# Kernel optimization log

Hardware: AMD Instinct MI355X
Metric: run time of the kernel (lower is better)

Reference implementation:

```python
import jax, jax.numpy as jnp
import numpy as np

K = 4  # recurrent_kernel_size


def setup_inputs() -> dict:
    key = jax.random.key(0)
    k1, k2, k3, k4 = jax.random.split(key, 4)
    b, t, d = 4, 4096, 1024
    x = jax.random.normal(k1, (b, t, d), dtype=jnp.float32)
    W_conv = jax.random.normal(k2, (d, 1, K), dtype=jnp.float32) * (1.0 / np.sqrt(K))
    W_proj = jax.random.normal(k3, (4 * d, d), dtype=jnp.float32) * (1.0 / np.sqrt(d))
    W_out = jax.random.normal(k4, (d, d), dtype=jnp.float32) * (1.0 / np.sqrt(d))
    return {"x": x, "W_conv": W_conv, "W_proj": W_proj, "W_out": W_out}


def _causal_dwconv(x_btd, W_conv):
    # x: [b,t,d]; W_conv: [d,1,k] (torch depthwise layout). Causal: left-pad k-1.
    d = x_btd.shape[-1]
    x_bdt = jnp.transpose(x_btd, (0, 2, 1))  # [b,d,t]
    y = jax.lax.conv_general_dilated(
        x_bdt, W_conv,
        window_strides=(1,),
        padding=[(K - 1, 0)],
        feature_group_count=d,
        dimension_numbers=("NCH", "OIH", "NCH"),
    )
    return jnp.transpose(y, (0, 2, 1))  # [b,t,d]


def reference(x, W_conv, W_proj, W_out):
    b, t, d = x.shape
    mixed = _causal_dwconv(x, W_conv)
    u = jnp.einsum("btd,ed->bte", x + mixed, W_proj)  # [b,t,4d]
    v, gate, decay, inject = jnp.split(u, 4, axis=-1)
    gate = jax.nn.sigmoid(gate)
    decay = jax.nn.sigmoid(decay)
    inject = jnp.tanh(inject)

    def step(state, inp):
        dec_t, inj_t, g_t, v_t = inp  # each [b,d]
        state = dec_t * state + (1.0 - dec_t) * inj_t
        out = g_t * v_t + (1.0 - g_t) * state
        return state, out

    # move time to leading axis for scan: [t,b,d]
    seq = (jnp.swapaxes(decay, 0, 1), jnp.swapaxes(inject, 0, 1),
           jnp.swapaxes(gate, 0, 1), jnp.swapaxes(v, 0, 1))
    state0 = jnp.zeros((b, d), dtype=x.dtype)
    _, y_tbd = jax.lax.scan(step, state0, seq)
    y = jnp.swapaxes(y_tbd, 0, 1)  # [b,t,d]
    return jnp.einsum("btd,ed->bte", y, W_out)
```

## Files before the change

### kernel.cpp

```cpp
#include <hip/hip_runtime.h>
#include <hip/hip_bf16.h>
#include <math.h>

typedef __hip_bfloat16 bf16;
typedef __bf16 bf16x8 __attribute__((ext_vector_type(8)));
typedef float f32x4 __attribute__((ext_vector_type(4)));
typedef float f32x4v __attribute__((ext_vector_type(4)));
typedef unsigned short u16x8v __attribute__((ext_vector_type(8)));
typedef unsigned short u16x4v __attribute__((ext_vector_type(4)));

#define AS1 __attribute__((address_space(1)))
#define AS3 __attribute__((address_space(3)))

#define BB 4
#define TT 4096
#define DD 1024

__device__ __forceinline__ float fast_sigmoid(float x) {
  return 1.0f / (1.0f + __expf(-x));
}
__device__ __forceinline__ float fast_tanh(float x) {
  return 2.0f / (1.0f + __expf(-2.0f * x)) - 1.0f;
}
__device__ __forceinline__ float b2f(unsigned short u) {
  union { unsigned int i; float f; } x;
  x.i = ((unsigned int)u) << 16;
  return x.f;
}
__device__ __forceinline__ unsigned short f2b(float f) {
  union { bf16 h; unsigned short u; } x;
  x.h = __float2bfloat16(f);
  return x.u;
}

__global__ __launch_bounds__(256) void w2bf_kernel(const float* __restrict__ w,
                                                   bf16* __restrict__ o,
                                                   int n) {
  int i = blockIdx.x * 256 + threadIdx.x;
  if (i < n) o[i] = __float2bfloat16(w[i]);
}

__global__ __launch_bounds__(256) void conv_add_kernel(
    const float* __restrict__ x, const float* __restrict__ Wc,
    bf16* __restrict__ xm, int total4) {
  int i = blockIdx.x * 256 + threadIdx.x;
  if (i >= total4) return;
  int c4 = (i & (DD / 4 - 1)) * 4;
  int t = (i / (DD / 4)) % TT;
  size_t base = (size_t)i * 4;
  f32x4v x0 = *(const f32x4v*)(x + base);
  f32x4v p1 = (t >= 1) ? *(const f32x4v*)(x + base - DD) : (f32x4v)0.0f;
  f32x4v p2 = (t >= 2) ? *(const f32x4v*)(x + base - 2 * DD) : (f32x4v)0.0f;
  f32x4v p3 = (t >= 3) ? *(const f32x4v*)(x + base - 3 * DD) : (f32x4v)0.0f;
  u16x4v o;
#pragma unroll
  for (int j = 0; j < 4; ++j) {
    f32x4v w = *(const f32x4v*)(Wc + (size_t)(c4 + j) * 4);
    float acc = x0[j] + w[3] * x0[j] + w[2] * p1[j] + w[1] * p2[j] +
                w[0] * p3[j];
    o[j] = f2b(acc);
  }
  *(u16x4v*)(xm + base) = o;
}

template <int EP>
__global__ __launch_bounds__(256, 4) void gemm128_kernel(
    const bf16* __restrict__ A, const bf16* __restrict__ B,
    void* __restrict__ C, int M, int N, int K, int MB) {
  __shared__ __align__(16) bf16 As[2][128][32];
  __shared__ __align__(16) bf16 Bs[2][128][32];

  const int tid = threadIdx.x;
  const int wv = tid >> 6, l = tid & 63;
  const int wm = wv >> 1, wn = wv & 1;

  const int bid = blockIdx.x;
  const int xcd = bid & 7, ii = bid >> 3;
  const int mb8 = MB >> 3;
  const int bm = xcd * mb8 + (ii % mb8);
  const int bn = ii / mb8;
  const int m0 = bm * 128, n0 = bn * 128;

  const int srow = l >> 2;
  const int scolE = ((l & 3) ^ ((l >> 2) & 3)) * 8;
  const bf16* Ab = A + (size_t)(m0 + wv * 32 + srow) * K + scolE;
  const bf16* Bb = B + (size_t)(n0 + wv * 32 + srow) * K + scolE;

  const int l15 = l & 15;
  const int physColB = ((l >> 4) ^ (l & 3)) * 16;
  const char* AsB = (const char*)As;
  const char* BsB = (const char*)Bs;
  const int aBase = wm * 4096 + l15 * 64 + physColB;
  const int bBase = wn * 4096 + l15 * 64 + physColB;

  auto stageKt = [&](int kt, int slot) {
    const int k0 = kt * 32;
#pragma unroll
    for (int j = 0; j < 2; ++j) {
      __builtin_amdgcn_global_load_lds(
          (const AS1 void*)(Ab + (size_t)(j * 16) * K + k0),
          (AS3 void*)&As[slot][wv * 32 + j * 16][0], 16, 0, 0);
      __builtin_amdgcn_global_load_lds(
          (const AS1 void*)(Bb + (size_t)(j * 16) * K + k0),
          (AS3 void*)&Bs[slot][wv * 32 + j * 16][0], 16, 0, 0);
    }
  };

  f32x4 acc[4][4];
#pragma unroll
  for (int i = 0; i < 4; ++i)
#pragma unroll
    for (int j = 0; j < 4; ++j) acc[i][j] = (f32x4)0.0f;

  const int NT = K >> 5;

  stageKt(0, 0);
  stageKt(1, 1);
  asm volatile("s_waitcnt vmcnt(4)" ::: "memory");
  __builtin_amdgcn_s_barrier();

  bf16x8 aF[4], bF[4];

#pragma unroll 1
  for (int t = 0; t < NT / 2; ++t) {
#pragma unroll
    for (int s = 0; s < 2; ++s) {
      const int kt = 2 * t + s;
      const int sof = s * 8192;
#pragma unroll
      for (int mi = 0; mi < 4; ++mi)
        aF[mi] = *(const bf16x8*)(AsB + aBase + sof + mi * 1024);
#pragma unroll
      for (int nj = 0; nj < 4; ++nj)
        bF[nj] = *(const bf16x8*)(BsB + bBase + sof + nj * 1024);
      __builtin_amdgcn_sched_barrier(0);
      __builtin_amdgcn_s_barrier();
      __builtin_amdgcn_s_setprio(1);
#pragma unroll
      for (int mi = 0; mi < 4; ++mi)
#pragma unroll
        for (int nj = 0; nj < 4; ++nj)
          acc[mi][nj] = __builtin_amdgcn_mfma_f32_16x16x32_bf16(
              aF[mi], bF[nj], acc[mi][nj], 0, 0, 0);
      __builtin_amdgcn_s_setprio(0);
      if (kt + 2 < NT) stageKt(kt + 2, s);
      if (kt + 1 < NT) {
        if (kt + 2 < NT)
          asm volatile("s_waitcnt vmcnt(4)" ::: "memory");
        else
          asm volatile("s_waitcnt vmcnt(0)" ::: "memory");
      }
      __builtin_amdgcn_sched_barrier(0);
      __builtin_amdgcn_s_barrier();
    }
  }

#pragma unroll
  for (int mi = 0; mi < 4; ++mi) {
    const int row = m0 + wm * 64 + mi * 16 + (l >> 4) * 4;
#pragma unroll
    for (int nj = 0; nj < 4; ++nj) {
      const int col = n0 + wn * 64 + nj * 16 + l15;
#pragma unroll
      for (int j = 0; j < 4; ++j) {
        float v = acc[mi][nj][j];
        if (EP == 0) {
          ((float*)C)[(size_t)(row + j) * N + col] = v;
        } else {
          const int cls = col >> 10;
          if (cls == 1 || cls == 2) v = fast_sigmoid(v);
          else if (cls == 3) v = fast_tanh(v);
          ((bf16*)C)[(size_t)(row + j) * N + col] = __float2bfloat16(v);
        }
      }
    }
  }
}

#define BM 64
#define BN 64
#define BKK 16
__global__ __launch_bounds__(256) void gemm_nt_kernel(
    const bf16* __restrict__ A, const float* __restrict__ B,
    float* __restrict__ C, int M, int N, int K) {
  __shared__ float Asm[BKK][BM + 1];
  __shared__ float Bsm[BKK][BN + 1];
  const int n0 = blockIdx.x * BN;
  const int m0 = blockIdx.y * BM;
  const int tid = threadIdx.x;
  const int tx = tid & 15, ty = tid >> 4;
  const int lk = tid & 15, lr = tid >> 4;
  float acc[4][4] = {};
  for (int k0 = 0; k0 < K; k0 += BKK) {
#pragma unroll
    for (int p = 0; p < 4; ++p) {
      Asm[lk][lr + 16 * p] =
          __bfloat162float(A[(size_t)(m0 + lr + 16 * p) * K + (k0 + lk)]);
      Bsm[lk][lr + 16 * p] = B[(size_t)(n0 + lr + 16 * p) * K + (k0 + lk)];
    }
    __syncthreads();
#pragma unroll
    for (int kk = 0; kk < BKK; ++kk) {
      float a[4], b[4];
#pragma unroll
      for (int i = 0; i < 4; ++i) a[i] = Asm[kk][ty * 4 + i];
#pragma unroll
      for (int j = 0; j < 4; ++j) b[j] = Bsm[kk][tx * 4 + j];
#pragma unroll
      for (int i = 0; i < 4; ++i)
#pragma unroll
        for (int j = 0; j < 4; ++j) acc[i][j] += a[i] * b[j];
    }
    __syncthreads();
  }
#pragma unroll
  for (int i = 0; i < 4; ++i)
#pragma unroll
    for (int j = 0; j < 4; ++j)
      C[(size_t)(m0 + ty * 4 + i) * N + (n0 + tx * 4 + j)] = acc[i][j];
}

__global__ __launch_bounds__(256) void scan_chunk_kernel(
    const bf16* __restrict__ u, float* __restrict__ cA,
    float* __restrict__ cB, int nchunk, int tchunk) {
  int idx = blockIdx.x * 256 + threadIdx.x;
  int c8 = (idx & (DD / 8 - 1)) * 8;
  int chunk = (idx / (DD / 8)) % nchunk;
  int b = idx / ((DD / 8) * nchunk);
  const bf16* ub = u + (size_t)b * TT * 4 * DD;
  float Aacc[8], Bacc[8];
#pragma unroll
  for (int j = 0; j < 8; ++j) { Aacc[j] = 1.0f; Bacc[j] = 0.0f; }
  int t0 = chunk * tchunk;
  for (int t = t0; t < t0 + tchunk; ++t) {
    const bf16* row = ub + (size_t)t * 4 * DD;
    u16x8v dv = *(const u16x8v*)(row + 2 * DD + c8);
    u16x8v iv = *(const u16x8v*)(row + 3 * DD + c8);
#pragma unroll
    for (int j = 0; j < 8; ++j) {
      float dec = b2f(dv[j]), inj = b2f(iv[j]);
      Aacc[j] *= dec;
      Bacc[j] = dec * Bacc[j] + (1.0f - dec) * inj;
    }
  }
  int base = (b * nchunk + chunk) * DD + c8;
#pragma unroll
  for (int j = 0; j < 8; ++j) { cA[base + j] = Aacc[j]; cB[base + j] = Bacc[j]; }
}

__global__ __launch_bounds__(256) void scan_prefix_kernel(
    const float* __restrict__ cA, const float* __restrict__ cB,
    float* __restrict__ S, int nchunk) {
  int idx = blockIdx.x * 256 + threadIdx.x;
  int c = idx % DD;
  int b = idx / DD;
  float s = 0.0f;
  for (int j = 0; j < nchunk; ++j) {
    int e = (b * nchunk + j) * DD + c;
    S[e] = s;
    s = cA[e] * s + cB[e];
  }
}

__global__ __launch_bounds__(256) void scan_out_kernel(
    const bf16* __restrict__ u, const float* __restrict__ S,
    bf16* __restrict__ y, int nchunk, int tchunk) {
  int idx = blockIdx.x * 256 + threadIdx.x;
  int c8 = (idx & (DD / 8 - 1)) * 8;
  int chunk = (idx / (DD / 8)) % nchunk;
  int b = idx / ((DD / 8) * nchunk);
  const bf16* ub = u + (size_t)b * TT * 4 * DD;
  bf16* yb = y + (size_t)b * TT * DD;
  float st[8];
  int sbase = (b * nchunk + chunk) * DD + c8;
#pragma unroll
  for (int j = 0; j < 8; ++j) st[j] = S[sbase + j];
  int t0 = chunk * tchunk;
  for (int t = t0; t < t0 + tchunk; ++t) {
    const bf16* row = ub + (size_t)t * 4 * DD;
    u16x8v vv = *(const u16x8v*)(row + c8);
    u16x8v gv = *(const u16x8v*)(row + DD + c8);
    u16x8v dv = *(const u16x8v*)(row + 2 * DD + c8);
    u16x8v iv = *(const u16x8v*)(row + 3 * DD + c8);
    u16x8v ov;
#pragma unroll
    for (int j = 0; j < 8; ++j) {
      float dec = b2f(dv[j]), inj = b2f(iv[j]);
      float g = b2f(gv[j]), v = b2f(vv[j]);
      st[j] = dec * st[j] + (1.0f - dec) * inj;
      ov[j] = f2b(g * v + (1.0f - g) * st[j]);
    }
    *(u16x8v*)(yb + (size_t)t * DD + c8) = ov;
  }
}

extern "C" void kernel_launch(void* const* d_in, const int* in_sizes, int n_in,
                              void* d_out, int out_size, void* d_ws,
                              size_t ws_size, hipStream_t stream) {
  const float* x = (const float*)d_in[0];
  const float* Wc = (const float*)d_in[1];
  const float* Wp = (const float*)d_in[2];
  const float* Wo = (const float*)d_in[3];
  float* out = (float*)d_out;

  const size_t nb = (size_t)TT * DD;

  auto need = [&](int nbat, int nchunk, bool wob) -> size_t {
    return (size_t)nbat * nb * 2 + (size_t)nbat * 4 * nb * 2 +
           (size_t)4 * DD * DD * 2 + (wob ? (size_t)DD * DD * 2 : 0) +
           (size_t)3 * nbat * nchunk * DD * 4;
  };

  int nbat, nchunk;
  bool haveWob;
  if (ws_size >= need(4, 64, true)) {
    nbat = 4; nchunk = 64; haveWob = true;
  } else if (ws_size >= need(1, 64, true)) {
    nbat = 1; nchunk = 64; haveWob = true;
  } else {
    nbat = 1; nchunk = 16; haveWob = false;
  }
  const int tchunk = TT / nchunk;

  char* p = (char*)d_ws;
  bf16* Wpb = (bf16*)p;  p += (size_t)4 * DD * DD * 2;
  bf16* Wob = nullptr;
  if (haveWob) { Wob = (bf16*)p; p += (size_t)DD * DD * 2; }
  bf16* xm = (bf16*)p;   p += (size_t)nbat * nb * 2;
  bf16* u = (bf16*)p;    p += (size_t)nbat * 4 * nb * 2;
  float* cA = (float*)p; p += (size_t)nbat * nchunk * DD * 4;
  float* cB = (float*)p; p += (size_t)nbat * nchunk * DD * 4;
  float* S = (float*)p;
  bf16* y = xm;

  w2bf_kernel<<<(4 * DD * DD) / 256, 256, 0, stream>>>(Wp, Wpb, 4 * DD * DD);
  if (haveWob)
    w2bf_kernel<<<(DD * DD) / 256, 256, 0, stream>>>(Wo, Wob, DD * DD);

  for (int b0 = 0; b0 < BB; b0 += nbat) {
    const float* xb = x + (size_t)b0 * nb;
    float* outb = out + (size_t)b0 * nb;
    const int Mtot = nbat * TT;
    const int total4 = (int)(nbat * nb / 4);

    conv_add_kernel<<<total4 / 256, 256, 0, stream>>>(xb, Wc, xm, total4);

    {
      const int MB = Mtot / 128;
      const int nwg = MB * (4 * DD / 128);
      gemm128_kernel<1><<<nwg, 256, 0, stream>>>(xm, Wpb, u, Mtot, 4 * DD, DD,
                                                 MB);
    }
    {
      int nthreads = nbat * nchunk * (DD / 8);
      scan_chunk_kernel<<<nthreads / 256, 256, 0, stream>>>(u, cA, cB, nchunk,
                                                            tchunk);
      scan_prefix_kernel<<<(nbat * DD) / 256, 256, 0, stream>>>(cA, cB, S,
                                                                nchunk);
      scan_out_kernel<<<nthreads / 256, 256, 0, stream>>>(u, S, y, nchunk,
                                                          tchunk);
    }
    if (haveWob) {
      const int MB = Mtot / 128;
      const int nwg = MB * (DD / 128);
      gemm128_kernel<0><<<nwg, 256, 0, stream>>>(y, Wob, outb, Mtot, DD, DD,
                                                 MB);
    } else {
      dim3 grid(DD / BN, Mtot / BM);
      gemm_nt_kernel<<<grid, 256, 0, stream>>>(y, Wo, outb, Mtot, DD, DD);
    }
  }
}
```

Before: 342.2 us.

## Replace double-buffered BK=32 GEMM pipeline with single-buffered BK=64 loop

After: 370.8 us. +8.4%, slower.

```diff
diff --git a/kernel.cpp b/kernel.cpp
--- a/kernel.cpp
+++ b/kernel.cpp
@@ -64,11 +64,11 @@
 }
 
 template <int EP>
-__global__ __launch_bounds__(256, 4) void gemm128_kernel(
+__global__ __launch_bounds__(256) void gemm128_kernel(
     const bf16* __restrict__ A, const bf16* __restrict__ B,
     void* __restrict__ C, int M, int N, int K, int MB) {
-  __shared__ __align__(16) bf16 As[2][128][32];
-  __shared__ __align__(16) bf16 Bs[2][128][32];
+  __shared__ __align__(16) bf16 As[128][64];
+  __shared__ __align__(16) bf16 Bs[128][64];
 
   const int tid = threadIdx.x;
   const int wv = tid >> 6, l = tid & 63;
@@ -81,78 +81,66 @@
   const int bn = ii / mb8;
   const int m0 = bm * 128, n0 = bn * 128;
 
-  const int srow = l >> 2;
-  const int scolE = ((l & 3) ^ ((l >> 2) & 3)) * 8;
-  const bf16* Ab = A + (size_t)(m0 + wv * 32 + srow) * K + scolE;
-  const bf16* Bb = B + (size_t)(n0 + wv * 32 + srow) * K + scolE;
+  const int lr3 = l >> 3;
+  const int scolE = ((l & 7) ^ lr3) * 8;
+  const bf16* Ab = A + (size_t)(m0 + wv * 32 + lr3) * K + scolE;
+  const bf16* Bb = B + (size_t)(n0 + wv * 32 + lr3) * K + scolE;
 
   const int l15 = l & 15;
-  const int physColB = ((l >> 4) ^ (l & 3)) * 16;
+  const int lh = l >> 4;
   const char* AsB = (const char*)As;
   const char* BsB = (const char*)Bs;
-  const int aBase = wm * 4096 + l15 * 64 + physColB;
-  const int bBase = wn * 4096 + l15 * 64 + physColB;
-
-  auto stageKt = [&](int kt, int slot) {
-    const int k0 = kt * 32;
-#pragma unroll
-    for (int j = 0; j < 2; ++j) {
+
+  f32x4 acc[4][4];
+#pragma unroll
+  for (int i = 0; i < 4; ++i)
+#pragma unroll
+    for (int j = 0; j < 4; ++j) acc[i][j] = (f32x4)0.0f;
+
+  const int NT = K >> 6;
+
+#pragma unroll 1
+  for (int kt = 0; kt < NT; ++kt) {
+    const int k0 = kt * 64;
+#pragma unroll
+    for (int j = 0; j < 4; ++j) {
       __builtin_amdgcn_global_load_lds(
-          (const AS1 void*)(Ab + (size_t)(j * 16) * K + k0),
-          (AS3 void*)&As[slot][wv * 32 + j * 16][0], 16, 0, 0);
+          (const AS1 void*)(Ab + (size_t)(j * 8) * K + k0),
+          (AS3 void*)&As[wv * 32 + j * 8][0], 16, 0, 0);
       __builtin_amdgcn_global_load_lds(
-          (const AS1 void*)(Bb + (size_t)(j * 16) * K + k0),
-          (AS3 void*)&Bs[slot][wv * 32 + j * 16][0], 16, 0, 0);
-    }
-  };
-
-  f32x4 acc[4][4];
-#pragma unroll
-  for (int i = 0; i < 4; ++i)
-#pragma unroll
-    for (int j = 0; j < 4; ++j) acc[i][j] = (f32x4)0.0f;
-
-  const int NT = K >> 5;
-
-  stageKt(0, 0);
-  stageKt(1, 1);
-  asm volatile("s_waitcnt vmcnt(4)" ::: "memory");
-  __builtin_amdgcn_s_barrier();
-
-  bf16x8 aF[4], bF[4];
-
-#pragma unroll 1
-  for (int t = 0; t < NT / 2; ++t) {
-#pragma unroll
-    for (int s = 0; s < 2; ++s) {
-      const int kt = 2 * t + s;
-      const int sof = s * 8192;
-#pragma unroll
-      for (int mi = 0; mi < 4; ++mi)
-        aF[mi] = *(const bf16x8*)(AsB + aBase + sof + mi * 1024);
-#pragma unroll
-      for (int nj = 0; nj < 4; ++nj)
-        bF[nj] = *(const bf16x8*)(BsB + bBase + sof + nj * 1024);
-      __builtin_amdgcn_sched_barrier(0);
-      __builtin_amdgcn_s_barrier();
-      __builtin_amdgcn_s_setprio(1);
+          (const AS1 void*)(Bb + (size_t)(j * 8) * K + k0),
+          (AS3 void*)&Bs[wv * 32 + j * 8][0], 16, 0, 0);
+    }
+    __syncthreads();
+
+    bf16x8 aF[4][2], bF[4][2];
+#pragma unroll
+    for (int mi = 0; mi < 4; ++mi) {
+      const int row = wm * 64 + mi * 16 + l15;
+#pragma unroll
+      for (int ks = 0; ks < 2; ++ks) {
+        const int ps = (ks * 4 + lh) ^ (l15 & 7);
+        aF[mi][ks] = *(const bf16x8*)(AsB + row * 128 + ps * 16);
+      }
+    }
+#pragma unroll
+    for (int nj = 0; nj < 4; ++nj) {
+      const int row = wn * 64 + nj * 16 + l15;
+#pragma unroll
+      for (int ks = 0; ks < 2; ++ks) {
+        const int ps = (ks * 4 + lh) ^ (l15 & 7);
+        bF[nj][ks] = *(const bf16x8*)(BsB + row * 128 + ps * 16);
+      }
+    }
+#pragma unroll
+    for (int ks = 0; ks < 2; ++ks)
 #pragma unroll
       for (int mi = 0; mi < 4; ++mi)
 #pragma unroll
         for (int nj = 0; nj < 4; ++nj)
           acc[mi][nj] = __builtin_amdgcn_mfma_f32_16x16x32_bf16(
-              aF[mi], bF[nj], acc[mi][nj], 0, 0, 0);
-      __builtin_amdgcn_s_setprio(0);
-      if (kt + 2 < NT) stageKt(kt + 2, s);
-      if (kt + 1 < NT) {
-        if (kt + 2 < NT)
-          asm volatile("s_waitcnt vmcnt(4)" ::: "memory");
-        else
-          asm volatile("s_waitcnt vmcnt(0)" ::: "memory");
-      }
-      __builtin_amdgcn_sched_barrier(0);
-      __builtin_amdgcn_s_barrier();
-    }
+              aF[mi][ks], bF[nj][ks], acc[mi][nj], 0, 0, 0);
+    __syncthreads();
   }
 
 #pragma unroll
```
